# Performance work log

Hardware: AMD Instinct MI355X
Metric: run time of the kernel (lower is better)

Reference implementation:

```python
import jax, jax.numpy as jnp
import numpy as np

B, M, N = 256, 512, 8192  # batch, N_v measurements, N_theta unknowns


def setup_inputs() -> dict:
    key = jax.random.key(0)
    ks = jax.random.split(key, 4)
    r_n = jax.random.normal(ks[0], (B, 2, N), jnp.float32)
    y = jax.random.normal(ks[1], (B, 2, M), jnp.float32)
    u_in = jax.random.normal(ks[2], (B, 2, M), jnp.float32)
    A = jax.random.normal(ks[3], (2, M, N), jnp.float32) / np.float32(np.sqrt(N))
    return {
        "r_n": r_n,
        "y": y,
        "u_in": u_in,
        "A": A,
        "log_rho": jnp.float32(0.0),
        "log_epsilon": jnp.float32(-2.3),
        "n_steps": 5,
    }


def reference(r_n, y, u_in, A, log_rho, log_epsilon, n_steps):
    rho = jnp.exp(jnp.clip(log_rho, -5.0, 5.0))
    eps = jnp.exp(jnp.clip(log_epsilon, -5.0, 0.0))
    Ar, Ai = A[0], A[1]  # [M, N]
    Mm = Ar.shape[0]

    def Amv(v):  # complex A @ v: [B,2,N] -> [B,2,M]
        vr, vi = v[:, 0], v[:, 1]
        o_r = jnp.einsum('mn,bn->bm', Ar, vr) - jnp.einsum('mn,bn->bm', Ai, vi)
        o_i = jnp.einsum('mn,bn->bm', Ar, vi) + jnp.einsum('mn,bn->bm', Ai, vr)
        return jnp.stack([o_r, o_i], axis=1)

    def AHmv(v):  # complex A^H @ v: [B,2,M] -> [B,2,N]
        vr, vi = v[:, 0], v[:, 1]
        o_r = jnp.einsum('mn,bm->bn', Ar, vr) + jnp.einsum('mn,bm->bn', Ai, vi)
        o_i = jnp.einsum('mn,bm->bn', Ar, vi) - jnp.einsum('mn,bm->bn', Ai, vr)
        return jnp.stack([o_r, o_i], axis=1)

    # SMW system S = (1/rho) I_M + A A^H as a real 2Mx2M block matrix.
    # It is identical across ADMM iterations, so build it once.
    I_M = jnp.eye(Mm, dtype=A.dtype)
    S_r = I_M / (rho + 1e-12) + Ar @ Ar.T + Ai @ Ai.T
    S_i = Ai @ Ar.T - Ar @ Ai.T
    S_block = jnp.block([[S_r, -S_i], [S_i, S_r]])  # [2M, 2M]

    u = u_in
    z = y
    x = r_n
    for _ in range(int(n_steps)):
        b = r_n + rho * AHmv(z - u)          # [B,2,N]
        Ab = Amv(b)                           # [B,2,M]
        R = jnp.concatenate([Ab[:, 0], Ab[:, 1]], axis=1)  # [B, 2M]
        T_flat = jnp.linalg.solve(S_block, R.T).T           # [B, 2M]
        T = jnp.stack([T_flat[:, :Mm], T_flat[:, Mm:]], axis=1)  # [B,2,M]
        x = b - AHmv(T)
        # enforce_positivity then enforce_real
        x = jnp.stack([jnp.maximum(x[:, 0], 0.0), jnp.zeros_like(x[:, 1])], axis=1)
        Ax = Amv(x)
        d = Ax + u - y
        nrm = jnp.sqrt(jnp.sum(d * d, axis=(1, 2), keepdims=True))
        scale = jnp.minimum(jnp.float32(1.0), eps / jnp.maximum(nrm, 1e-12))
        z = y + scale * d  # projection of d onto eps-ball around 0, recentered at y
        u = u + Ax - z
    return x, u
```

## Files before the change

kernel.cpp:

```cpp
#include <hip/hip_runtime.h>


typedef __attribute__((ext_vector_type(8))) short short8;
typedef __attribute__((ext_vector_type(8))) unsigned short ushort8;
typedef __attribute__((ext_vector_type(4))) float floatx4;

__device__ __forceinline__ unsigned short f2bf(float x) {
    unsigned u = __float_as_uint(x);
    u += 0x7fffu + ((u >> 16) & 1u);
    return (unsigned short)(u >> 16);
}
__device__ __forceinline__ float bf2f(unsigned short h) {
    return __uint_as_float(((unsigned)h) << 16);
}

__device__ __forceinline__ int aswz(int row, int col) {
    return col ^ (((row >> 3) & 7) << 3);
}

__device__ __forceinline__ void gld16(const unsigned short* g, unsigned short* s) {
    __builtin_amdgcn_global_load_lds(
        (const __attribute__((address_space(1))) void*)g,
        (__attribute__((address_space(3))) void*)s, 16, 0, 0);
}

template<int MT, int CF, int AMODE, int BMODE, bool RELU, int DMODE,
         bool IMINUS, bool ZIMAG>
__global__ __launch_bounds__(256) void gemm_bf16(
    const void* __restrict__ Ap, int lda,
    const void* __restrict__ Bp, int ldb,
    const float* __restrict__ Df, int ldd, float beta,
    const unsigned short* __restrict__ Db, int lddb,
    float* __restrict__ Cf, int ldcf,
    unsigned short* __restrict__ Cb, int ldcb,
    long czoff, int K)
{
    constexpr bool GLD = (AMODE == 0 && BMODE == 0);
    constexpr int LDW  = GLD ? 64 : 72;
    constexpr int BN  = CF * 32;
    constexpr int WR  = (MT == 256) ? 4 : 2;
    constexpr int WC  = 4 / WR;
    constexpr int RPW = MT / WR;
    constexpr int RF  = RPW / 16;
    constexpr int CPW = BN / WC;
    constexpr int CFW = CPW / 16;

    __shared__ unsigned short As[MT][LDW];
    __shared__ unsigned short Bs[BN][LDW];

    const int tid = threadIdx.x, wave = tid >> 6, lane = tid & 63;
    const int brow = blockIdx.y * MT;
    const int bcol = blockIdx.x * BN;
    const int bzk  = blockIdx.z;
    const int kbeg = bzk * K;
    const int sr = tid >> 3, sk = (tid & 7) << 3;
    const int wr = wave / WC, wc = wave % WC;
    const int l15 = lane & 15, quad = lane >> 4, fk = quad << 3;
    const int gl_row = lane >> 3;
    const int gl_src = ((lane & 7) ^ gl_row) << 3;

    floatx4 acc[RF][CFW];
    #pragma unroll
    for (int i = 0; i < RF; i++)
        #pragma unroll
        for (int j = 0; j < CFW; j++) acc[i][j] = (floatx4){0.f, 0.f, 0.f, 0.f};

    if (Cf) Cf += (size_t)bzk * czoff;
    if (Cb) Cb += (size_t)bzk * czoff;

    for (int k0 = kbeg; k0 < kbeg + K; k0 += 64) {
        if constexpr (GLD) {
            const unsigned short* Ab = (const unsigned short*)Ap;
            const unsigned short* Bb = (const unsigned short*)Bp;
            #pragma unroll
            for (int h = 0; h < MT / 32; h++) {
                const int rb = (h * 4 + wave) * 8;
                gld16(Ab + (size_t)(brow + rb + gl_row) * lda + (k0 + gl_src),
                      &As[rb][0]);
            }
            #pragma unroll
            for (int h = 0; h < BN / 32; h++) {
                const int rb = (h * 4 + wave) * 8;
                gld16(Bb + (size_t)(bcol + rb + gl_row) * ldb + (k0 + gl_src),
                      &Bs[rb][0]);
            }
        } else {
            if (AMODE == 3) {
                const unsigned short* Gb = (const unsigned short*)Ap;
                #pragma unroll
                for (int h = 0; h < MT / 32; h++) {
                    const int kr = sr + 32 * (h & 1);
                    const int cb = sk + 64 * (h >> 1);
                    const int kc = aswz(cb, kr);
                    const ushort8 v =
                        *(const ushort8*)(Gb + (size_t)(k0 + kr) * lda + (brow + cb));
                    As[cb+0][kc]=v[0]; As[cb+1][kc]=v[1];
                    As[cb+2][kc]=v[2]; As[cb+3][kc]=v[3];
                    As[cb+4][kc]=v[4]; As[cb+5][kc]=v[5];
                    As[cb+6][kc]=v[6]; As[cb+7][kc]=v[7];
                }
            } else {
                const unsigned short* Ab = (const unsigned short*)Ap;
                #pragma unroll
                for (int h = 0; h < MT / 32; h++) {
                    const int r = sr + h * 32;
                    *(ushort8*)&As[r][aswz(r, sk)] =
                        *(const ushort8*)(Ab + (size_t)(brow + r) * lda + (k0 + sk));
                }
            }
            {
                const unsigned short* Bb = (const unsigned short*)Bp;
                #pragma unroll
                for (int h = 0; h < BN / 32; h++) {
                    const int r = sr + h * 32;
                    *(ushort8*)&Bs[r][sk] =
                        *(const ushort8*)(Bb + (size_t)(bcol + r) * ldb + (k0 + sk));
                }
            }
        }
        __syncthreads();
        #pragma unroll
        for (int s = 0; s < 2; s++) {
            short8 af[RF];
            #pragma unroll
            for (int rf = 0; rf < RF; rf++) {
                const int ar = wr * RPW + rf * 16 + l15;
                const int ac = GLD ? (((s << 5) + fk) ^ ((ar & 7) << 3))
                                   : aswz(ar, (s << 5) + fk);
                af[rf] = *(const short8*)&As[ar][ac];
            }
            #pragma unroll
            for (int c = 0; c < CFW; c++) {
                const int br = wc * CPW + c * 16 + l15;
                const int bc = GLD ? (((s << 5) + fk) ^ ((br & 7) << 3))
                                   : ((s << 5) + fk);
                const short8 bf = *(const short8*)&Bs[br][bc];
                #pragma unroll
                for (int rf = 0; rf < RF; rf++)
                    acc[rf][c] = __builtin_amdgcn_mfma_f32_16x16x32_bf16(af[rf], bf, acc[rf][c], 0, 0, 0);
            }
        }
        __syncthreads();
    }

    const int r0 = brow + wr * RPW + (quad << 2);
    const int c0 = bcol + wc * CPW + l15;
    #pragma unroll
    for (int rf = 0; rf < RF; rf++) {
        #pragma unroll
        for (int c = 0; c < CFW; c++) {
            #pragma unroll
            for (int reg = 0; reg < 4; reg++) {
                const int row = r0 + rf * 16 + reg;
                const int col = c0 + c * 16;
                float v = acc[rf][c][reg];
                if (IMINUS) v = ((row == col) ? 1.f : 0.f) - v;
                if (DMODE == 1) v = fmaf(beta, Df[(size_t)row * ldd + col], v);
                if (DMODE == 2) v = v + bf2f(Db[(size_t)row * lddb + col]);
                if (RELU) v = fmaxf(v, 0.f);
                if (Cf) {
                    Cf[(size_t)row * ldcf + col] = v;
                    if (ZIMAG) Cf[(size_t)row * ldcf + 8192 + col] = 0.f;
                }
                if (Cb) Cb[(size_t)row * ldcb + col] = f2bf(v);
            }
        }
    }
}


__global__ __launch_bounds__(256) void castA_k(const float* __restrict__ A,
    unsigned short* __restrict__ Ab)
{
    const int idx = blockIdx.x * 256 + threadIdx.x;
    const float4 f0 = ((const float4*)A)[2 * idx];
    const float4 f1 = ((const float4*)A)[2 * idx + 1];
    ushort8 v;
    v[0]=f2bf(f0.x); v[1]=f2bf(f0.y); v[2]=f2bf(f0.z); v[3]=f2bf(f0.w);
    v[4]=f2bf(f1.x); v[5]=f2bf(f1.y); v[6]=f2bf(f1.z); v[7]=f2bf(f1.w);
    ((ushort8*)Ab)[idx] = v;
}

__global__ __launch_bounds__(256) void assemble_k(const float* __restrict__ Gp,
    unsigned short* __restrict__ Sbf, float* __restrict__ rowsum,
    const float* __restrict__ log_rho)
{
    const int i = blockIdx.x, t = threadIdx.x;
    const float rho = expf(fminf(fmaxf(log_rho[0], -5.f), 5.f));
    const float eps = 1.f / (rho + 1e-12f);
    float a = 0.f;
    #pragma unroll
    for (int k = 0; k < 4; k++) {
        const int j = t + k * 256;
        const int idx = (i << 10) | j;
        const int idx2 = (((i + 512) & 1023) << 10) | ((j + 512) & 1023);
        float g = 0.f, g2 = 0.f;
        #pragma unroll
        for (int p = 0; p < 4; p++) {
            g  += Gp[idx  + p * 1048576];
            g2 += Gp[idx2 + p * 1048576];
        }
        const float sgn = ((i < 512) == (j < 512)) ? 1.f : -1.f;
        const float s = g + sgn * g2 + ((i == j) ? eps : 0.f);
        Sbf[idx] = f2bf(s);
        a += fabsf(s);
    }
    #pragma unroll
    for (int off = 32; off > 0; off >>= 1) a += __shfl_down(a, off);
    __shared__ float red[4];
    if ((t & 63) == 0) red[t >> 6] = a;
    __syncthreads();
    if (t == 0) rowsum[i] = ((red[0] + red[1]) + (red[2] + red[3]));
}

__global__ void lam_k(float* rowsum) {
    float m = 0.f;
    for (int i = threadIdx.x; i < 1024; i += 256) m = fmaxf(m, rowsum[i]);
    #pragma unroll
    for (int off = 32; off > 0; off >>= 1) m = fmaxf(m, __shfl_down(m, off));
    __shared__ float red[4];
    if ((threadIdx.x & 63) == 0) red[threadIdx.x >> 6] = m;
    __syncthreads();
    if (threadIdx.x == 0) rowsum[1024] = fmaxf(fmaxf(red[0], red[1]), fmaxf(red[2], red[3]));
}

__global__ __launch_bounds__(256) void initx_k(unsigned short* __restrict__ X,
    const float* __restrict__ rowsum, const float* __restrict__ log_rho)
{
    const int idx = blockIdx.x * 256 + threadIdx.x;
    const int i = idx >> 10, j = idx & 1023;
    const float rho = expf(fminf(fmaxf(log_rho[0], -5.f), 5.f));
    const float eps = 1.f / (rho + 1e-12f);
    X[idx] = (i == j) ? f2bf(2.f / (rowsum[1024] + eps)) : (unsigned short)0;
}

__global__ __launch_bounds__(256) void recarn_k(const float* __restrict__ P2,
    const float* __restrict__ y, unsigned short* __restrict__ rhs0c,
    const float* __restrict__ log_rho)
{
    const int idx = blockIdx.x * 256 + threadIdx.x;
    const int b = idx >> 9, j = idx & 511;
    float rr = 0.f, ir = 0.f, ri = 0.f, ii = 0.f;
    #pragma unroll
    for (int p = 0; p < 4; p++) {
        const float* pr = P2 + (size_t)p * 524288 + (size_t)(2 * b) * 1024;
        const float* pi = pr + 1024;
        rr += pr[j]; ir += pr[512 + j];
        ri += pi[j]; ii += pi[512 + j];
    }
    const float arn_r = rr - ii;
    const float arn_i = ri + ir;
    const float rho = expf(fminf(fmaxf(log_rho[0], -5.f), 5.f));
    const float er = rho / (rho + 1e-12f);
    rhs0c[b * 1024 + j]       = f2bf(er * y[b * 1024 + j]       - arn_r);
    rhs0c[b * 1024 + 512 + j] = f2bf(er * y[b * 1024 + 512 + j] - arn_i);
}

__global__ __launch_bounds__(256) void initrhs_k(const float* __restrict__ u_in,
    const unsigned short* __restrict__ rhs0c, unsigned short* __restrict__ rhs,
    float* __restrict__ u, const float* __restrict__ log_rho)
{
    const int idx = blockIdx.x * 256 + threadIdx.x;
    const float rho = expf(fminf(fmaxf(log_rho[0], -5.f), 5.f));
    const float er = rho / (rho + 1e-12f);
    u[idx] = u_in[idx];
    rhs[idx] = f2bf(bf2f(rhs0c[idx]) - er * u_in[idx]);
}

__global__ __launch_bounds__(256) void update_k(const unsigned short* __restrict__ Axp,
    const float* __restrict__ y, float* __restrict__ u,
    const unsigned short* __restrict__ rhs0c, unsigned short* __restrict__ rhs,
    const float* __restrict__ log_rho, const float* __restrict__ log_eps,
    int writerhs)
{
    const int b = blockIdx.x, t = threadIdx.x;
    const unsigned short* a0 = Axp + b * 1024;
    const float* yb = y + b * 1024;
    float* ub = u + b * 1024;
    float d[4]; float s = 0.f;
    #pragma unroll
    for (int r = 0; r < 4; r++) {
        const int e = t + r * 256;
        float dd = ub[e] - yb[e];
        #pragma unroll
        for (int p = 0; p < 4; p++) dd += bf2f(a0[e + p * 262144]);
        d[r] = dd; s = fmaf(dd, dd, s);
    }
    #pragma unroll
    for (int off = 32; off > 0; off >>= 1) s += __shfl_down(s, off);
    __shared__ float red[4];
    if ((t & 63) == 0) red[t >> 6] = s;
    __syncthreads();
    const float tot = ((red[0] + red[1]) + (red[2] + red[3]));
    const float eps = expf(fminf(fmaxf(log_eps[0], -5.f), 0.f));
    const float scale = fminf(1.f, eps / fmaxf(sqrtf(tot), 1e-12f));
    const float rho = expf(fminf(fmaxf(log_rho[0], -5.f), 5.f));
    const float er = rho / (rho + 1e-12f);
    #pragma unroll
    for (int r = 0; r < 4; r++) {
        const int e = t + r * 256;
        ub[e] = (1.f - scale) * d[r];
        if (writerhs)
            rhs[b * 1024 + e] = f2bf(bf2f(rhs0c[b * 1024 + e])
                                     + er * (2.f * scale - 1.f) * d[r]);
    }
}

extern "C" void kernel_launch(void* const* d_in, const int* in_sizes, int n_in,
                              void* d_out, int out_size, void* d_ws, size_t ws_size,
                              hipStream_t stream)
{
    const float* r_n     = (const float*)d_in[0];
    const float* y       = (const float*)d_in[1];
    const float* u_in    = (const float*)d_in[2];
    const float* A       = (const float*)d_in[3];
    const float* log_rho = (const float*)d_in[4];
    const float* log_eps = (const float*)d_in[5];

    char* wsb = (char*)d_ws;
    float*          Gp    = (float*)wsb;
    float*          P2    = (float*)wsb;
    unsigned short* rn_bf = (unsigned short*)(wsb + (8u << 20));
    unsigned short* Wt    = (unsigned short*)wsb;
    unsigned short* Sbf   = (unsigned short*)(wsb + (16u << 20));
    unsigned short* Xa    = (unsigned short*)(wsb + (18u << 20));
    unsigned short* Xb    = (unsigned short*)(wsb + (20u << 20));
    unsigned short* Rbf   = (unsigned short*)(wsb + (22u << 20));
    unsigned short* xbf   = (unsigned short*)(wsb + (16u << 20));
    unsigned short* Axp   = (unsigned short*)(wsb + (20u << 20));
    unsigned short* rhs0c = (unsigned short*)(wsb + (22u << 20));
    unsigned short* rhsbf = (unsigned short*)(wsb + (22u << 20) + (512u << 10));
    float*          rowsum= (float*)(wsb + (23u << 20));

    float* out_x = (float*)d_out;
    float* out_u = out_x + 256 * 2 * 8192;
    unsigned short* A_bf = (unsigned short*)d_out;

    castA_k<<<4096,256,0,stream>>>(A, A_bf);

    gemm_bf16<64,2,0,0,false,0,false,false><<<dim3(16,16,4),256,0,stream>>>(
        A_bf,8192, A_bf,8192, nullptr,0,0.f, nullptr,0,
        Gp,1024, nullptr,0, 1048576, 2048);
    assemble_k<<<1024,256,0,stream>>>(Gp, Sbf, rowsum, log_rho);
    castA_k<<<2048,256,0,stream>>>(r_n, rn_bf);
    lam_k<<<1,256,0,stream>>>(rowsum);
    initx_k<<<4096,256,0,stream>>>(Xa, rowsum, log_rho);

    gemm_bf16<32,2,0,0,false,0,false,false><<<dim3(16,16,4),256,0,stream>>>(
        rn_bf,8192, A_bf,8192, nullptr,0,0.f, nullptr,0,
        P2,1024, nullptr,0, 524288, 2048);

    unsigned short* xa = Xa; unsigned short* xb = Xb;
    for (int it = 0; it < 5; it++) {
        gemm_bf16<32,1,0,0,false,0,true,false><<<dim3(32,32,1),256,0,stream>>>(
            Sbf,1024, xa,1024, nullptr,0,0.f, nullptr,0,
            nullptr,0, Rbf,1024, 0, 1024);
        gemm_bf16<32,1,0,0,false,2,false,false><<<dim3(32,32,1),256,0,stream>>>(
            xa,1024, Rbf,1024, nullptr,0,0.f, xa,1024,
            nullptr,0, xb,1024, 0, 1024);
        unsigned short* t = xa; xa = xb; xb = t;
    }
    const unsigned short* Sinv = xa;

    recarn_k<<<512,256,0,stream>>>(P2, y, rhs0c, log_rho);
    initrhs_k<<<1024,256,0,stream>>>(u_in, rhs0c, rhsbf, out_u, log_rho);

    gemm_bf16<64,8,3,0,false,0,false,false><<<dim3(4,128,1),256,0,stream>>>(
        A_bf,8192, Sinv,1024, nullptr,0,0.f, nullptr,0,
        nullptr,0, Wt,1024, 0, 1024);

    for (int it = 0; it < 5; it++) {
        gemm_bf16<64,1,0,0,true,1,false,false><<<dim3(256,4,1),256,0,stream>>>(
            rhsbf,1024, Wt,1024, r_n,16384,1.f, nullptr,0,
            nullptr,0, xbf,8192, 0, 1024);
        gemm_bf16<32,1,0,0,false,0,false,false><<<dim3(32,8,4),256,0,stream>>>(
            xbf,8192, A_bf,8192, nullptr,0,0.f, nullptr,0,
            nullptr,0, Axp,1024, 262144, 2048);
        update_k<<<256,256,0,stream>>>(Axp, y, out_u, rhs0c, rhsbf,
                                       log_rho, log_eps, (it < 4) ? 1 : 0);
    }

    gemm_bf16<64,1,0,0,true,1,false,true><<<dim3(256,4,1),256,0,stream>>>(
        rhsbf,1024, Wt,1024, r_n,16384,1.f, nullptr,0,
        out_x,16384, nullptr,0, 0, 1024);
}
```

Measured before the change: 511.6 us.

## Exploit symmetry in Gram GEMM and block structure in Newton-Schulz inverse

The Gram matrix GEMM (A_bf·A_bfᵀ) now computes only the lower-triangular tiles, and assemble_k reads the mirrored element for the upper triangle. The Newton–Schulz iterations for the SMW inverse launch half the row tiles and write each result tile twice: once in place and once into the complementary quadrant with a sign flip. This uses the [[P,-Q],[Q,P]] structure of real-encoded complex matrices. Together these roughly halve the GEMM work in the setup phase, at the cost of scattered mirrored stores and idle early-exit blocks.

After: 538.9 us. 1.05x slower.

```diff
diff --git a/kernel.cpp b/kernel.cpp
--- a/kernel.cpp
+++ b/kernel.cpp
@@ -25,7 +25,7 @@
 }
 
 template<int MT, int CF, int AMODE, int BMODE, bool RELU, int DMODE,
-         bool IMINUS, bool ZIMAG>
+         bool IMINUS, bool ZIMAG, bool TRIL, bool MIRROR>
 __global__ __launch_bounds__(256) void gemm_bf16(
     const void* __restrict__ Ap, int lda,
     const void* __restrict__ Bp, int ldb,
@@ -35,6 +35,8 @@
     unsigned short* __restrict__ Cb, int ldcb,
     long czoff, int K)
 {
+    if (TRIL && blockIdx.x > blockIdx.y) return;
+
     constexpr bool GLD = (AMODE == 0 && BMODE == 0);
     constexpr int LDW  = GLD ? 64 : 72;
     constexpr int BN  = CF * 32;
@@ -162,7 +164,14 @@
                     Cf[(size_t)row * ldcf + col] = v;
                     if (ZIMAG) Cf[(size_t)row * ldcf + 8192 + col] = 0.f;
                 }
-                if (Cb) Cb[(size_t)row * ldcb + col] = f2bf(v);
+                if (Cb) {
+                    const unsigned short b = f2bf(v);
+                    Cb[(size_t)row * ldcb + col] = b;
+                    if (MIRROR)
+                        Cb[(size_t)(row + 512) * ldcb + ((col + 512) & 1023)] =
+                            b ^ ((col >= 512) ? (unsigned short)0x8000
+                                              : (unsigned short)0);
+                }
             }
         }
     }
@@ -192,17 +201,18 @@
     #pragma unroll
     for (int k = 0; k < 4; k++) {
         const int j = t + k * 256;
-        const int idx = (i << 10) | j;
-        const int idx2 = (((i + 512) & 1023) << 10) | ((j + 512) & 1023);
+        const int a1 = (j <= i) ? ((i << 10) | j) : ((j << 10) | i);
+        const int r2 = (i + 512) & 1023, c2 = (j + 512) & 1023;
+        const int a2 = (c2 <= r2) ? ((r2 << 10) | c2) : ((c2 << 10) | r2);
         float g = 0.f, g2 = 0.f;
         #pragma unroll
         for (int p = 0; p < 4; p++) {
-            g  += Gp[idx  + p * 1048576];
-            g2 += Gp[idx2 + p * 1048576];
+            g  += Gp[a1 + p * 1048576];
+            g2 += Gp[a2 + p * 1048576];
         }
         const float sgn = ((i < 512) == (j < 512)) ? 1.f : -1.f;
         const float s = g + sgn * g2 + ((i == j) ? eps : 0.f);
-        Sbf[idx] = f2bf(s);
+        Sbf[(i << 10) | j] = f2bf(s);
         a += fabsf(s);
     }
     #pragma unroll
@@ -338,7 +348,7 @@
 
     castA_k<<<4096,256,0,stream>>>(A, A_bf);
 
-    gemm_bf16<64,2,0,0,false,0,false,false><<<dim3(16,16,4),256,0,stream>>>(
+    gemm_bf16<64,2,0,0,false,0,false,false,true,false><<<dim3(16,16,4),256,0,stream>>>(
         A_bf,8192, A_bf,8192, nullptr,0,0.f, nullptr,0,
         Gp,1024, nullptr,0, 1048576, 2048);
     assemble_k<<<1024,256,0,stream>>>(Gp, Sbf, rowsum, log_rho);
@@ -346,16 +356,16 @@
     lam_k<<<1,256,0,stream>>>(rowsum);
     initx_k<<<4096,256,0,stream>>>(Xa, rowsum, log_rho);
 
-    gemm_bf16<32,2,0,0,false,0,false,false><<<dim3(16,16,4),256,0,stream>>>(
+    gemm_bf16<32,2,0,0,false,0,false,false,false,false><<<dim3(16,16,4),256,0,stream>>>(
         rn_bf,8192, A_bf,8192, nullptr,0,0.f, nullptr,0,
         P2,1024, nullptr,0, 524288, 2048);
 
     unsigned short* xa = Xa; unsigned short* xb = Xb;
     for (int it = 0; it < 5; it++) {
-        gemm_bf16<32,1,0,0,false,0,true,false><<<dim3(32,32,1),256,0,stream>>>(
+        gemm_bf16<32,1,0,0,false,0,true,false,false,true><<<dim3(32,16,1),256,0,stream>>>(
             Sbf,1024, xa,1024, nullptr,0,0.f, nullptr,0,
             nullptr,0, Rbf,1024, 0, 1024);
-        gemm_bf16<32,1,0,0,false,2,false,false><<<dim3(32,32,1),256,0,stream>>>(
+        gemm_bf16<32,1,0,0,false,2,false,false,false,true><<<dim3(32,16,1),256,0,stream>>>(
             xa,1024, Rbf,1024, nullptr,0,0.f, xa,1024,
             nullptr,0, xb,1024, 0, 1024);
         unsigned short* t = xa; xa = xb; xb = t;
@@ -365,22 +375,22 @@
     recarn_k<<<512,256,0,stream>>>(P2, y, rhs0c, log_rho);
     initrhs_k<<<1024,256,0,stream>>>(u_in, rhs0c, rhsbf, out_u, log_rho);
 
-    gemm_bf16<64,8,3,0,false,0,false,false><<<dim3(4,128,1),256,0,stream>>>(
+    gemm_bf16<64,8,3,0,false,0,false,false,false,false><<<dim3(4,128,1),256,0,stream>>>(
         A_bf,8192, Sinv,1024, nullptr,0,0.f, nullptr,0,
         nullptr,0, Wt,1024, 0, 1024);
 
     for (int it = 0; it < 5; it++) {
-        gemm_bf16<64,1,0,0,true,1,false,false><<<dim3(256,4,1),256,0,stream>>>(
+        gemm_bf16<64,1,0,0,true,1,false,false,false,false><<<dim3(256,4,1),256,0,stream>>>(
             rhsbf,1024, Wt,1024, r_n,16384,1.f, nullptr,0,
             nullptr,0, xbf,8192, 0, 1024);
-        gemm_bf16<32,1,0,0,false,0,false,false><<<dim3(32,8,4),256,0,stream>>>(
+        gemm_bf16<32,1,0,0,false,0,false,false,false,false><<<dim3(32,8,4),256,0,stream>>>(
             xbf,8192, A_bf,8192, nullptr,0,0.f, nullptr,0,
             nullptr,0, Axp,1024, 262144, 2048);
         update_k<<<256,256,0,stream>>>(Axp, y, out_u, rhs0c, rhsbf,
                                        log_rho, log_eps, (it < 4) ? 1 : 0);
     }
 
-    gemm_bf16<64,1,0,0,true,1,false,true><<<dim3(256,4,1),256,0,stream>>>(
+    gemm_bf16<64,1,0,0,true,1,false,true,false,false><<<dim3(256,4,1),256,0,stream>>>(
         rhsbf,1024, Wt,1024, r_n,16384,1.f, nullptr,0,
         out_x,16384, nullptr,0, 0, 1024);
 }
```

## Double-buffer LDS tiles in async global-load GEMM path

Applied to the files above, without the earlier changes.

For the GEMM variant that loads A and B tiles straight into LDS with global_load_lds, the tile buffers become two-deep. The next k-tile is issued while MFMAs run on the current one, and only one barrier per iteration remains instead of two. This should hide global memory latency behind compute, at the cost of double the LDS for those instantiations, which may lower occupancy.

After: 523.6 us. 2.3% more time.

```diff
diff --git a/kernel.cpp b/kernel.cpp
--- a/kernel.cpp
+++ b/kernel.cpp
@@ -37,6 +37,7 @@
 {
     constexpr bool GLD = (AMODE == 0 && BMODE == 0);
     constexpr int LDW  = GLD ? 64 : 72;
+    constexpr int NBUF = GLD ? 2 : 1;
     constexpr int BN  = CF * 32;
     constexpr int WR  = (MT == 256) ? 4 : 2;
     constexpr int WC  = 4 / WR;
@@ -45,8 +46,8 @@
     constexpr int CPW = BN / WC;
     constexpr int CFW = CPW / 16;
 
-    __shared__ unsigned short As[MT][LDW];
-    __shared__ unsigned short Bs[BN][LDW];
+    __shared__ unsigned short As[NBUF][MT][LDW];
+    __shared__ unsigned short Bs[NBUF][BN][LDW];
 
     const int tid = threadIdx.x, wave = tid >> 6, lane = tid & 63;
     const int brow = blockIdx.y * MT;
@@ -68,23 +69,59 @@
     if (Cf) Cf += (size_t)bzk * czoff;
     if (Cb) Cb += (size_t)bzk * czoff;
 
-    for (int k0 = kbeg; k0 < kbeg + K; k0 += 64) {
-        if constexpr (GLD) {
-            const unsigned short* Ab = (const unsigned short*)Ap;
-            const unsigned short* Bb = (const unsigned short*)Bp;
+    auto compute = [&](int b) {
+        #pragma unroll
+        for (int s = 0; s < 2; s++) {
+            short8 af[RF];
+            #pragma unroll
+            for (int rf = 0; rf < RF; rf++) {
+                const int ar = wr * RPW + rf * 16 + l15;
+                const int ac = GLD ? (((s << 5) + fk) ^ ((ar & 7) << 3))
+                                   : aswz(ar, (s << 5) + fk);
+                af[rf] = *(const short8*)&As[b][ar][ac];
+            }
+            #pragma unroll
+            for (int c = 0; c < CFW; c++) {
+                const int br = wc * CPW + c * 16 + l15;
+                const int bc = GLD ? (((s << 5) + fk) ^ ((br & 7) << 3))
+                                   : ((s << 5) + fk);
+                const short8 bf = *(const short8*)&Bs[b][br][bc];
+                #pragma unroll
+                for (int rf = 0; rf < RF; rf++)
+                    acc[rf][c] = __builtin_amdgcn_mfma_f32_16x16x32_bf16(af[rf], bf, acc[rf][c], 0, 0, 0);
+            }
+        }
+    };
+
+    if constexpr (GLD) {
+        const unsigned short* Ab = (const unsigned short*)Ap;
+        const unsigned short* Bb = (const unsigned short*)Bp;
+        auto stage = [&](int b, int k0) {
             #pragma unroll
             for (int h = 0; h < MT / 32; h++) {
                 const int rb = (h * 4 + wave) * 8;
                 gld16(Ab + (size_t)(brow + rb + gl_row) * lda + (k0 + gl_src),
-                      &As[rb][0]);
+                      &As[b][rb][0]);
             }
             #pragma unroll
             for (int h = 0; h < BN / 32; h++) {
                 const int rb = (h * 4 + wave) * 8;
                 gld16(Bb + (size_t)(bcol + rb + gl_row) * ldb + (k0 + gl_src),
-                      &Bs[rb][0]);
-            }
-        } else {
+                      &Bs[b][rb][0]);
+            }
+        };
+        stage(0, kbeg);
+        __syncthreads();
+        int cur = 0;
+        for (int k0 = kbeg; k0 < kbeg + K; k0 += 64) {
+            const bool more = (k0 + 64 < kbeg + K);
+            if (more) stage(cur ^ 1, k0 + 64);
+            compute(cur);
+            if (more) __syncthreads();
+            cur ^= 1;
+        }
+    } else {
+        for (int k0 = kbeg; k0 < kbeg + K; k0 += 64) {
             if (AMODE == 3) {
                 const unsigned short* Gb = (const unsigned short*)Ap;
                 #pragma unroll
@@ -94,17 +131,17 @@
                     const int kc = aswz(cb, kr);
                     const ushort8 v =
                         *(const ushort8*)(Gb + (size_t)(k0 + kr) * lda + (brow + cb));
-                    As[cb+0][kc]=v[0]; As[cb+1][kc]=v[1];
-                    As[cb+2][kc]=v[2]; As[cb+3][kc]=v[3];
-                    As[cb+4][kc]=v[4]; As[cb+5][kc]=v[5];
-                    As[cb+6][kc]=v[6]; As[cb+7][kc]=v[7];
+                    As[0][cb+0][kc]=v[0]; As[0][cb+1][kc]=v[1];
+                    As[0][cb+2][kc]=v[2]; As[0][cb+3][kc]=v[3];
+                    As[0][cb+4][kc]=v[4]; As[0][cb+5][kc]=v[5];
+                    As[0][cb+6][kc]=v[6]; As[0][cb+7][kc]=v[7];
                 }
             } else {
                 const unsigned short* Ab = (const unsigned short*)Ap;
                 #pragma unroll
                 for (int h = 0; h < MT / 32; h++) {
                     const int r = sr + h * 32;
-                    *(ushort8*)&As[r][aswz(r, sk)] =
+                    *(ushort8*)&As[0][r][aswz(r, sk)] =
                         *(const ushort8*)(Ab + (size_t)(brow + r) * lda + (k0 + sk));
                 }
             }
@@ -113,34 +150,14 @@
                 #pragma unroll
                 for (int h = 0; h < BN / 32; h++) {
                     const int r = sr + h * 32;
-                    *(ushort8*)&Bs[r][sk] =
+                    *(ushort8*)&Bs[0][r][sk] =
                         *(const ushort8*)(Bb + (size_t)(bcol + r) * ldb + (k0 + sk));
                 }
             }
+            __syncthreads();
+            compute(0);
+            __syncthreads();
         }
-        __syncthreads();
-        #pragma unroll
-        for (int s = 0; s < 2; s++) {
-            short8 af[RF];
-            #pragma unroll
-            for (int rf = 0; rf < RF; rf++) {
-                const int ar = wr * RPW + rf * 16 + l15;
-                const int ac = GLD ? (((s << 5) + fk) ^ ((ar & 7) << 3))
-                                   : aswz(ar, (s << 5) + fk);
-                af[rf] = *(const short8*)&As[ar][ac];
-            }
-            #pragma unroll
-            for (int c = 0; c < CFW; c++) {
-                const int br = wc * CPW + c * 16 + l15;
-                const int bc = GLD ? (((s << 5) + fk) ^ ((br & 7) << 3))
-                                   : ((s << 5) + fk);
-                const short8 bf = *(const short8*)&Bs[br][bc];
-                #pragma unroll
-                for (int rf = 0; rf < RF; rf++)
-                    acc[rf][c] = __builtin_amdgcn_mfma_f32_16x16x32_bf16(af[rf], bf, acc[rf][c], 0, 0, 0);
-            }
-        }
-        __syncthreads();
     }
 
     const int r0 = brow + wr * RPW + (quad << 2);
```
